# Kernel optimization log

Hardware: AMD Instinct MI355X
Metric: run time of the kernel (lower is better)

Reference implementation:

```python
import jax, jax.numpy as jnp
import numpy as np

N_NODES = 100000


def setup_inputs() -> dict:
    key = jax.random.key(0)
    k1, k2, k3, k4, k5 = jax.random.split(key, 5)
    n_feat, n_class = 128, 64
    E = 3200000
    x = jax.random.normal(k1, (N_NODES, n_feat), dtype=jnp.float32)
    edge_index = jax.random.randint(k2, (2, E), 0, N_NODES, dtype=jnp.int64)
    edge_weight = jax.random.uniform(k3, (E,), dtype=jnp.float32)
    # GCNConv params: glorot weight [in, out], zero-init bias (use small random for a non-trivial check)
    limit = float(np.sqrt(6.0 / (n_feat + n_class)))
    W = jax.random.uniform(k4, (n_feat, n_class), dtype=jnp.float32, minval=-limit, maxval=limit)
    b = jax.random.normal(k5, (n_class,), dtype=jnp.float32) * 0.01
    return {"x": x, "edge_index": edge_index, "edge_weight": edge_weight, "W": W, "b": b}


def _gcn_norm(edge_index, edge_weight, n):
    # add self-loops with weight 1 (PyG default fill_value=1.0)
    loop = jnp.arange(n, dtype=edge_index.dtype)
    row = jnp.concatenate([edge_index[0], loop])
    col = jnp.concatenate([edge_index[1], loop])
    w = jnp.concatenate([edge_weight, jnp.ones((n,), dtype=edge_weight.dtype)])
    deg = jax.ops.segment_sum(w, col, num_segments=n)  # in-degree by weight
    dis = jnp.where(deg > 0, jax.lax.rsqrt(jnp.where(deg > 0, deg, 1.0)), 0.0)
    norm = dis[row] * w * dis[col]
    return row, col, norm


def reference(x, edge_index, edge_weight, W, b):
    n = x.shape[0]
    row, col, norm = _gcn_norm(edge_index, edge_weight, n)
    h = x @ W  # linear transform before propagation, as in PyG GCNConv
    # gather source messages, scale by norm, scatter-add into targets
    msgs = h[row] * norm[:, None]          # [E+N, n_class]
    out = jax.ops.segment_sum(msgs, col, num_segments=n)
    return jax.nn.sigmoid(out + b)
```

## Files before the change

kernel.cpp:

```cpp
#include <hip/hip_runtime.h>
#include <hip/hip_bf16.h>
#include <math.h>


#define BLK 256
#define BBLK 1024
#define ABLK 1024
#define NBINBLK 512
#define NGRP 8
#define NB  512
#define CAPG 1024
#define CPB_MAX 200
#define PAD 76

typedef unsigned long long u64;
typedef unsigned int u32;
typedef unsigned short u16;
typedef unsigned char u8;
typedef _Float16 half8 __attribute__((ext_vector_type(8)));
typedef float f32x4 __attribute__((ext_vector_type(4)));

__global__ __launch_bounds__(BLK) void k_prep(const float* __restrict__ W,
                                              u16* __restrict__ WT,
                                              u32* __restrict__ cursor) {
    int gid = blockIdx.x * BLK + threadIdx.x;
    int gsz = gridDim.x * BLK;
    for (int i = gid; i < NB * NGRP; i += gsz) cursor[i] = 0u;
    for (int i = gid; i < 64 * 128; i += gsz) {
        int nn = i >> 7, k = i & 127;
        _Float16 h = (_Float16)W[k * 64 + nn];
        WT[nn * 128 + k] = *(u16*)&h;
    }
}

__global__ __launch_bounds__(BBLK) void k_bin(const int* __restrict__ row,
                                              const int* __restrict__ col,
                                              const float* __restrict__ w,
                                              u32* cursor,
                                              u64* __restrict__ staged,
                                              int E, int cpb, int nbins, int bpb) {
    __shared__ u32 hist[NB];
    __shared__ u32 sbase[NB];
    int t = threadIdx.x;
    int grp = blockIdx.x & (NGRP - 1);
    for (int j = t; j < NB; j += BBLK) hist[j] = 0;
    __syncthreads();
    int e0 = blockIdx.x * bpb;
    int e1 = min(e0 + bpb, E);
    int e = e0 + t;
    for (; e + 3 * BBLK < e1; e += 4 * BBLK) {
        int c0 = col[e];
        int c1 = col[e + BBLK];
        int c2 = col[e + 2 * BBLK];
        int c3 = col[e + 3 * BBLK];
        atomicAdd(&hist[(u32)c0 / (u32)cpb], 1u);
        atomicAdd(&hist[(u32)c1 / (u32)cpb], 1u);
        atomicAdd(&hist[(u32)c2 / (u32)cpb], 1u);
        atomicAdd(&hist[(u32)c3 / (u32)cpb], 1u);
    }
    for (; e < e1; e += BBLK)
        atomicAdd(&hist[(u32)col[e] / (u32)cpb], 1u);
    __syncthreads();
    for (int j = t; j < nbins; j += BBLK) {
        u32 h = hist[j];
        sbase[j] = h ? atomicAdd(&cursor[j * NGRP + grp], h) : 0u;
        hist[j] = 0u;
    }
    __syncthreads();
    e = e0 + t;
    for (; e + 3 * BBLK < e1; e += 4 * BBLK) {
#pragma unroll
        for (int j = 0; j < 4; j++) {
            int ee = e + j * BBLK;
            u32 c = (u32)col[ee];
            u32 bin = c / (u32)cpb;
            u32 colrel = c - bin * (u32)cpb;
            u32 wfix = (u32)(w[ee] * 65535.0f + 0.5f);
            u32 rel = sbase[bin] + atomicAdd(&hist[bin], 1u);
            if (rel < (u32)CAPG)
                staged[((size_t)bin * NGRP + grp) * CAPG + rel] =
                    (u64)((u32)row[ee] & 0xFFFFFu) | ((u64)colrel << 20)
                    | ((u64)wfix << 32);
        }
    }
    for (; e < e1; e += BBLK) {
        u32 c = (u32)col[e];
        u32 bin = c / (u32)cpb;
        u32 colrel = c - bin * (u32)cpb;
        u32 wfix = (u32)(w[e] * 65535.0f + 0.5f);
        u32 rel = sbase[bin] + atomicAdd(&hist[bin], 1u);
        if (rel < (u32)CAPG)
            staged[((size_t)bin * NGRP + grp) * CAPG + rel] =
                (u64)((u32)row[e] & 0xFFFFFu) | ((u64)colrel << 20)
                | ((u64)wfix << 32);
    }
}

__global__ __launch_bounds__(BLK) void k_deg(const u32* __restrict__ cursor,
                                             const u64* __restrict__ staged,
                                             float* __restrict__ dis,
                                             int N, int cpb) {
    __shared__ u32 deg[CPB_MAX];
    int bin = blockIdx.x, t = threadIdx.x;
    if (t < CPB_MAX) deg[t] = 0u;
    __syncthreads();
    for (int g = 0; g < NGRP; g++) {
        int ne = min((int)cursor[bin * NGRP + g], CAPG);
        size_t base = ((size_t)bin * NGRP + g) * CAPG;
        for (int i = t; i < ne; i += BLK) {
            u64 s = staged[base + i];
            atomicAdd(&deg[(u32)(s >> 20) & 0xFFFu], (u32)(s >> 32));
        }
    }
    __syncthreads();
    for (int j = t; j < cpb; j += BLK) {
        int c = bin * cpb + j;
        if (c < N)
            dis[c] = rsqrtf(1.0f + (float)deg[j] * (1.0f / 65535.0f));
    }
}

static __device__ __forceinline__ u16 f2bf(float f) {
    __hip_bfloat16 h = __float2bfloat16(f);
    return *(u16*)&h;
}

__global__ __launch_bounds__(BLK) void k_gemmM(const float* __restrict__ x,
                                               const u16* __restrict__ WT,
                                               const float* __restrict__ dis,
                                               u16* __restrict__ hs, int n) {
    __shared__ __attribute__((aligned(16))) _Float16 sx[64 * 136];
    __shared__ __attribute__((aligned(16))) _Float16 sw[64 * 136];
    __shared__ float sdis[64];
    int t = threadIdx.x;
    int m0 = blockIdx.x * 64;
    for (int i = t; i < 2048; i += BLK) {
        int r = i >> 5, q = i & 31;
        int gr = m0 + r;
        float4 v = make_float4(0.f, 0.f, 0.f, 0.f);
        if (gr < n) v = ((const float4*)x)[(size_t)gr * 32 + q];
        _Float16* dst = &sx[r * 136 + q * 4];
        dst[0] = (_Float16)v.x; dst[1] = (_Float16)v.y;
        dst[2] = (_Float16)v.z; dst[3] = (_Float16)v.w;
    }
    for (int i = t; i < 2048; i += BLK) {
        int nn = i >> 5, q = i & 31;
        ushort4 v = ((const ushort4*)WT)[nn * 32 + q];
        u16* dst = (u16*)&sw[nn * 136 + q * 4];
        dst[0] = v.x; dst[1] = v.y; dst[2] = v.z; dst[3] = v.w;
    }
    if (t < 64) sdis[t] = (m0 + t < n) ? dis[m0 + t] : 0.f;
    __syncthreads();
    int wv = t >> 6, lane = t & 63;
    int quad = lane >> 4, l16 = lane & 15;
    int mrow = wv * 16 + l16;
    half8 af[4];
#pragma unroll
    for (int kt = 0; kt < 4; kt++)
        af[kt] = *(const half8*)&sx[mrow * 136 + kt * 32 + quad * 8];
#pragma unroll
    for (int n0t = 0; n0t < 4; n0t++) {
        f32x4 acc = {0.f, 0.f, 0.f, 0.f};
#pragma unroll
        for (int kt = 0; kt < 4; kt++) {
            half8 bf_ = *(const half8*)&sw[(n0t * 16 + l16) * 136 + kt * 32 + quad * 8];
            acc = __builtin_amdgcn_mfma_f32_16x16x32_f16(af[kt], bf_, acc, 0, 0, 0);
        }
#pragma unroll
        for (int r = 0; r < 4; r++) {
            int mr = wv * 16 + quad * 4 + r;
            int gr = m0 + mr;
            if (gr < n)
                hs[(size_t)gr * 64 + n0t * 16 + l16] = f2bf(acc[r] * sdis[mr]);
        }
    }
}

__global__ __launch_bounds__(ABLK) void k_buildagg(const u32* __restrict__ cursor,
                                                   const u64* __restrict__ staged,
                                                   const uint2* __restrict__ hs64,
                                                   const float* __restrict__ dis,
                                                   const float* __restrict__ b,
                                                   float* __restrict__ out,
                                                   int N, int cpb) {
    __shared__ u32 cnt[CPB_MAX];
    __shared__ u32 lbkt[CPB_MAX * PAD];
    int bin = blockIdx.x, t = threadIdx.x;
    if (t < CPB_MAX) cnt[t] = 0u;
    __syncthreads();
    for (int g = 0; g < NGRP; g++) {
        int ne = min((int)cursor[bin * NGRP + g], CAPG);
        size_t base = ((size_t)bin * NGRP + g) * CAPG;
        for (int i = t; i < ne; i += ABLK) {
            u64 s = staged[base + i];
            u32 colrel = (u32)(s >> 20) & 0xFFFu;
            u32 wfix = (u32)(s >> 32);
            u32 rk = atomicAdd(&cnt[colrel], 1u);
            if (rk < (u32)PAD)
                lbkt[colrel * PAD + rk] = ((u32)s & 0xFFFFFu) | ((wfix >> 1) << 17);
        }
    }
    __syncthreads();
    int wv = t >> 6;
    int lane = t & 63;
    int q = lane >> 4, fp = lane & 15;
    const float WS = 1.0f / 32767.0f;
    for (int colrel = wv; colrel < cpb; colrel += (ABLK / 64)) {
        int node = bin * cpb + colrel;
        if (node >= N) break;
        int cc = (int)cnt[colrel];
        if (cc > PAD) cc = PAD;
        const u32* bkt = &lbkt[colrel * PAD];
        float a0, a1, a2, a3;
        if (q == 0) {
            uint2 s = hs64[((size_t)node << 4) + fp];
            a0 = __uint_as_float(s.x << 16);
            a1 = __uint_as_float(s.x & 0xFFFF0000u);
            a2 = __uint_as_float(s.y << 16);
            a3 = __uint_as_float(s.y & 0xFFFF0000u);
        } else {
            a0 = a1 = a2 = a3 = 0.f;
        }
        for (int e = 0; e < cc; e += 4) {
            int idx = e + q;
            u32 p = (idx < cc) ? bkt[idx] : 0u;
            float w = (float)(p >> 17) * WS;
            uint2 g = hs64[((size_t)(p & 0x1FFFFu) << 4) + fp];
            a0 = fmaf(__uint_as_float(g.x << 16), w, a0);
            a1 = fmaf(__uint_as_float(g.x & 0xFFFF0000u), w, a1);
            a2 = fmaf(__uint_as_float(g.y << 16), w, a2);
            a3 = fmaf(__uint_as_float(g.y & 0xFFFF0000u), w, a3);
        }
        a0 += __shfl_down(a0, 16); a1 += __shfl_down(a1, 16);
        a2 += __shfl_down(a2, 16); a3 += __shfl_down(a3, 16);
        a0 += __shfl_down(a0, 32); a1 += __shfl_down(a1, 32);
        a2 += __shfl_down(a2, 32); a3 += __shfl_down(a3, 32);
        if (q == 0) {
            float d = dis[node];
            float4 bv = ((const float4*)b)[fp];
            float4 o;
            o.x = 1.0f / (1.0f + __expf(-(d * a0 + bv.x)));
            o.y = 1.0f / (1.0f + __expf(-(d * a1 + bv.y)));
            o.z = 1.0f / (1.0f + __expf(-(d * a2 + bv.z)));
            o.w = 1.0f / (1.0f + __expf(-(d * a3 + bv.w)));
            ((float4*)out)[((size_t)node << 4) + fp] = o;
        }
    }
}

static inline size_t align_up(size_t v, size_t a) { return (v + a - 1) & ~(a - 1); }

extern "C" void kernel_launch(void* const* d_in, const int* in_sizes, int n_in,
                              void* d_out, int out_size, void* d_ws, size_t ws_size,
                              hipStream_t stream) {
    const float* x  = (const float*)d_in[0];
    const int*   ei = (const int*)d_in[1];
    const float* ew = (const float*)d_in[2];
    const float* W  = (const float*)d_in[3];
    const float* b  = (const float*)d_in[4];
    float* out = (float*)d_out;

    const int E = in_sizes[2];
    const int N = in_sizes[0] / 128;

    const int* row = ei;
    const int* col = ei + E;

    const int cpb   = (N + NB - 1) / NB;
    const int nbins = (N + cpb - 1) / cpb;
    const int bpb   = (E + NBINBLK - 1) / NBINBLK;

    char* p = (char*)d_ws;
    u32* cursor = (u32*)p; p += align_up((size_t)NB * NGRP * 4, 256);
    u64* staged = (u64*)p; p += align_up((size_t)NB * NGRP * CAPG * 8, 256);
    float* dis  = (float*)p; p += align_up((size_t)N * 4, 256);
    u16* hs     = (u16*)p; p += align_up((size_t)N * 64 * 2, 256);
    u16* WT     = (u16*)p; p += align_up((size_t)64 * 128 * 2, 256);
    (void)ws_size;

    k_prep<<<8, BLK, 0, stream>>>(W, WT, cursor);
    k_bin<<<NBINBLK, BBLK, 0, stream>>>(row, col, ew, cursor, staged,
                                        E, cpb, nbins, bpb);
    k_deg<<<nbins, BLK, 0, stream>>>(cursor, staged, dis, N, cpb);
    k_gemmM<<<(N + 63) / 64, BLK, 0, stream>>>(x, WT, dis, hs, N);
    k_buildagg<<<nbins, ABLK, 0, stream>>>(cursor, staged, (const uint2*)hs,
                                           dis, b, out, N, cpb);
}
```

Baseline: 268.2 us.

## Fold degree computation into binning and apply source normalization in aggregation

Removes the separate degree kernel: k_bin now accumulates per-node weighted degree with global atomics, and the GEMM no longer scales rows by the source normalization. The aggregation kernel computes rsqrt of the source degree per staged edge when building its local buckets, folds it into the quantized edge weight, and applies the destination normalization itself. A memset replaces the cursor-zeroing loop, and launch_bounds adds an occupancy hint to the aggregation kernel. This trades one kernel launch and one pass over staged edges for millions of global atomics and random degree reads in aggregation, and quantizing the combined weight can change precision.

```diff
diff --git a/kernel.cpp b/kernel.cpp
--- a/kernel.cpp
+++ b/kernel.cpp
@@ -16,20 +16,72 @@
 typedef unsigned long long u64;
 typedef unsigned int u32;
 typedef unsigned short u16;
-typedef unsigned char u8;
 typedef _Float16 half8 __attribute__((ext_vector_type(8)));
 typedef float f32x4 __attribute__((ext_vector_type(4)));
 
+static __device__ __forceinline__ u16 f2bf(float f) {
+    __hip_bfloat16 h = __float2bfloat16(f);
+    return *(u16*)&h;
+}
+static __device__ __forceinline__ float bfl(u32 v) { return __uint_as_float(v << 16); }
+static __device__ __forceinline__ float bfh(u32 v) { return __uint_as_float(v & 0xFFFF0000u); }
+
 __global__ __launch_bounds__(BLK) void k_prep(const float* __restrict__ W,
-                                              u16* __restrict__ WT,
-                                              u32* __restrict__ cursor) {
+                                              u16* __restrict__ WT) {
     int gid = blockIdx.x * BLK + threadIdx.x;
     int gsz = gridDim.x * BLK;
-    for (int i = gid; i < NB * NGRP; i += gsz) cursor[i] = 0u;
     for (int i = gid; i < 64 * 128; i += gsz) {
         int nn = i >> 7, k = i & 127;
         _Float16 h = (_Float16)W[k * 64 + nn];
         WT[nn * 128 + k] = *(u16*)&h;
+    }
+}
+
+__global__ __launch_bounds__(BLK) void k_gemmU(const float* __restrict__ x,
+                                               const u16* __restrict__ WT,
+                                               u16* __restrict__ hs, int n) {
+    __shared__ __attribute__((aligned(16))) _Float16 sx[64 * 136];
+    __shared__ __attribute__((aligned(16))) _Float16 sw[64 * 136];
+    int t = threadIdx.x;
+    int m0 = blockIdx.x * 64;
+    for (int i = t; i < 2048; i += BLK) {
+        int r = i >> 5, q = i & 31;
+        int gr = m0 + r;
+        float4 v = make_float4(0.f, 0.f, 0.f, 0.f);
+        if (gr < n) v = ((const float4*)x)[(size_t)gr * 32 + q];
+        _Float16* dst = &sx[r * 136 + q * 4];
+        dst[0] = (_Float16)v.x; dst[1] = (_Float16)v.y;
+        dst[2] = (_Float16)v.z; dst[3] = (_Float16)v.w;
+    }
+    for (int i = t; i < 2048; i += BLK) {
+        int nn = i >> 5, q = i & 31;
+        ushort4 v = ((const ushort4*)WT)[nn * 32 + q];
+        u16* dst = (u16*)&sw[nn * 136 + q * 4];
+        dst[0] = v.x; dst[1] = v.y; dst[2] = v.z; dst[3] = v.w;
+    }
+    __syncthreads();
+    int wv = t >> 6, lane = t & 63;
+    int quad = lane >> 4, l16 = lane & 15;
+    int mrow = wv * 16 + l16;
+    half8 af[4];
+#pragma unroll
+    for (int kt = 0; kt < 4; kt++)
+        af[kt] = *(const half8*)&sx[mrow * 136 + kt * 32 + quad * 8];
+#pragma unroll
+    for (int n0t = 0; n0t < 4; n0t++) {
+        f32x4 acc = {0.f, 0.f, 0.f, 0.f};
+#pragma unroll
+        for (int kt = 0; kt < 4; kt++) {
+            half8 bf_ = *(const half8*)&sw[(n0t * 16 + l16) * 136 + kt * 32 + quad * 8];
+            acc = __builtin_amdgcn_mfma_f32_16x16x32_f16(af[kt], bf_, acc, 0, 0, 0);
+        }
+#pragma unroll
+        for (int r = 0; r < 4; r++) {
+            int mr = wv * 16 + quad * 4 + r;
+            int gr = m0 + mr;
+            if (gr < n)
+                hs[(size_t)gr * 64 + n0t * 16 + l16] = f2bf(acc[r]);
+        }
     }
 }
 
@@ -38,6 +90,7 @@
                                               const float* __restrict__ w,
                                               u32* cursor,
                                               u64* __restrict__ staged,
+                                              u32* __restrict__ deg,
                                               int E, int cpb, int nbins, int bpb) {
     __shared__ u32 hist[NB];
     __shared__ u32 sbase[NB];
@@ -76,6 +129,7 @@
             u32 bin = c / (u32)cpb;
             u32 colrel = c - bin * (u32)cpb;
             u32 wfix = (u32)(w[ee] * 65535.0f + 0.5f);
+            atomicAdd(&deg[c], wfix);
             u32 rel = sbase[bin] + atomicAdd(&hist[bin], 1u);
             if (rel < (u32)CAPG)
                 staged[((size_t)bin * NGRP + grp) * CAPG + rel] =
@@ -88,6 +142,7 @@
         u32 bin = c / (u32)cpb;
         u32 colrel = c - bin * (u32)cpb;
         u32 wfix = (u32)(w[e] * 65535.0f + 0.5f);
+        atomicAdd(&deg[c], wfix);
         u32 rel = sbase[bin] + atomicAdd(&hist[bin], 1u);
         if (rel < (u32)CAPG)
             staged[((size_t)bin * NGRP + grp) * CAPG + rel] =
@@ -96,95 +151,16 @@
     }
 }
 
-__global__ __launch_bounds__(BLK) void k_deg(const u32* __restrict__ cursor,
-                                             const u64* __restrict__ staged,
-                                             float* __restrict__ dis,
-                                             int N, int cpb) {
-    __shared__ u32 deg[CPB_MAX];
-    int bin = blockIdx.x, t = threadIdx.x;
-    if (t < CPB_MAX) deg[t] = 0u;
-    __syncthreads();
-    for (int g = 0; g < NGRP; g++) {
-        int ne = min((int)cursor[bin * NGRP + g], CAPG);
-        size_t base = ((size_t)bin * NGRP + g) * CAPG;
-        for (int i = t; i < ne; i += BLK) {
-            u64 s = staged[base + i];
-            atomicAdd(&deg[(u32)(s >> 20) & 0xFFFu], (u32)(s >> 32));
-        }
-    }
-    __syncthreads();
-    for (int j = t; j < cpb; j += BLK) {
-        int c = bin * cpb + j;
-        if (c < N)
-            dis[c] = rsqrtf(1.0f + (float)deg[j] * (1.0f / 65535.0f));
-    }
-}
-
-static __device__ __forceinline__ u16 f2bf(float f) {
-    __hip_bfloat16 h = __float2bfloat16(f);
-    return *(u16*)&h;
-}
-
-__global__ __launch_bounds__(BLK) void k_gemmM(const float* __restrict__ x,
-                                               const u16* __restrict__ WT,
-                                               const float* __restrict__ dis,
-                                               u16* __restrict__ hs, int n) {
-    __shared__ __attribute__((aligned(16))) _Float16 sx[64 * 136];
-    __shared__ __attribute__((aligned(16))) _Float16 sw[64 * 136];
-    __shared__ float sdis[64];
-    int t = threadIdx.x;
-    int m0 = blockIdx.x * 64;
-    for (int i = t; i < 2048; i += BLK) {
-        int r = i >> 5, q = i & 31;
-        int gr = m0 + r;
-        float4 v = make_float4(0.f, 0.f, 0.f, 0.f);
-        if (gr < n) v = ((const float4*)x)[(size_t)gr * 32 + q];
-        _Float16* dst = &sx[r * 136 + q * 4];
-        dst[0] = (_Float16)v.x; dst[1] = (_Float16)v.y;
-        dst[2] = (_Float16)v.z; dst[3] = (_Float16)v.w;
-    }
-    for (int i = t; i < 2048; i += BLK) {
-        int nn = i >> 5, q = i & 31;
-        ushort4 v = ((const ushort4*)WT)[nn * 32 + q];
-        u16* dst = (u16*)&sw[nn * 136 + q * 4];
-        dst[0] = v.x; dst[1] = v.y; dst[2] = v.z; dst[3] = v.w;
-    }
-    if (t < 64) sdis[t] = (m0 + t < n) ? dis[m0 + t] : 0.f;
-    __syncthreads();
-    int wv = t >> 6, lane = t & 63;
-    int quad = lane >> 4, l16 = lane & 15;
-    int mrow = wv * 16 + l16;
-    half8 af[4];
-#pragma unroll
-    for (int kt = 0; kt < 4; kt++)
-        af[kt] = *(const half8*)&sx[mrow * 136 + kt * 32 + quad * 8];
-#pragma unroll
-    for (int n0t = 0; n0t < 4; n0t++) {
-        f32x4 acc = {0.f, 0.f, 0.f, 0.f};
-#pragma unroll
-        for (int kt = 0; kt < 4; kt++) {
-            half8 bf_ = *(const half8*)&sw[(n0t * 16 + l16) * 136 + kt * 32 + quad * 8];
-            acc = __builtin_amdgcn_mfma_f32_16x16x32_f16(af[kt], bf_, acc, 0, 0, 0);
-        }
-#pragma unroll
-        for (int r = 0; r < 4; r++) {
-            int mr = wv * 16 + quad * 4 + r;
-            int gr = m0 + mr;
-            if (gr < n)
-                hs[(size_t)gr * 64 + n0t * 16 + l16] = f2bf(acc[r] * sdis[mr]);
-        }
-    }
-}
-
-__global__ __launch_bounds__(ABLK) void k_buildagg(const u32* __restrict__ cursor,
-                                                   const u64* __restrict__ staged,
-                                                   const uint2* __restrict__ hs64,
-                                                   const float* __restrict__ dis,
-                                                   const float* __restrict__ b,
-                                                   float* __restrict__ out,
-                                                   int N, int cpb) {
+__global__ __launch_bounds__(ABLK, 8) void k_agg(const u32* __restrict__ cursor,
+                                                 const u64* __restrict__ staged,
+                                                 const uint2* __restrict__ hs64,
+                                                 const u32* __restrict__ deg,
+                                                 const float* __restrict__ b,
+                                                 float* __restrict__ out,
+                                                 int N, int cpb) {
     __shared__ u32 cnt[CPB_MAX];
     __shared__ u32 lbkt[CPB_MAX * PAD];
+    const float DS = 1.0f / 65535.0f;
     int bin = blockIdx.x, t = threadIdx.x;
     if (t < CPB_MAX) cnt[t] = 0u;
     __syncthreads();
@@ -194,10 +170,13 @@
         for (int i = t; i < ne; i += ABLK) {
             u64 s = staged[base + i];
             u32 colrel = (u32)(s >> 20) & 0xFFFu;
-            u32 wfix = (u32)(s >> 32);
+            u32 rowid = (u32)s & 0xFFFFFu;
+            float dr = rsqrtf(1.0f + (float)deg[rowid] * DS);
+            float wp = (float)(u32)(s >> 32) * DS * dr;
+            u32 q15 = (u32)(wp * 32767.0f + 0.5f);
             u32 rk = atomicAdd(&cnt[colrel], 1u);
             if (rk < (u32)PAD)
-                lbkt[colrel * PAD + rk] = ((u32)s & 0xFFFFFu) | ((wfix >> 1) << 17);
+                lbkt[colrel * PAD + rk] = rowid | (q15 << 17);
         }
     }
     __syncthreads();
@@ -211,13 +190,14 @@
         int cc = (int)cnt[colrel];
         if (cc > PAD) cc = PAD;
         const u32* bkt = &lbkt[colrel * PAD];
+        float dnode = rsqrtf(1.0f + (float)deg[node] * DS);
         float a0, a1, a2, a3;
         if (q == 0) {
             uint2 s = hs64[((size_t)node << 4) + fp];
-            a0 = __uint_as_float(s.x << 16);
-            a1 = __uint_as_float(s.x & 0xFFFF0000u);
-            a2 = __uint_as_float(s.y << 16);
-            a3 = __uint_as_float(s.y & 0xFFFF0000u);
+            a0 = bfl(s.x) * dnode;
+            a1 = bfh(s.x) * dnode;
+            a2 = bfl(s.y) * dnode;
+            a3 = bfh(s.y) * dnode;
         } else {
             a0 = a1 = a2 = a3 = 0.f;
         }
@@ -226,23 +206,22 @@
             u32 p = (idx < cc) ? bkt[idx] : 0u;
             float w = (float)(p >> 17) * WS;
             uint2 g = hs64[((size_t)(p & 0x1FFFFu) << 4) + fp];
-            a0 = fmaf(__uint_as_float(g.x << 16), w, a0);
-            a1 = fmaf(__uint_as_float(g.x & 0xFFFF0000u), w, a1);
-            a2 = fmaf(__uint_as_float(g.y << 16), w, a2);
-            a3 = fmaf(__uint_as_float(g.y & 0xFFFF0000u), w, a3);
+            a0 = fmaf(bfl(g.x), w, a0);
+            a1 = fmaf(bfh(g.x), w, a1);
+            a2 = fmaf(bfl(g.y), w, a2);
+            a3 = fmaf(bfh(g.y), w, a3);
         }
         a0 += __shfl_down(a0, 16); a1 += __shfl_down(a1, 16);
         a2 += __shfl_down(a2, 16); a3 += __shfl_down(a3, 16);
         a0 += __shfl_down(a0, 32); a1 += __shfl_down(a1, 32);
         a2 += __shfl_down(a2, 32); a3 += __shfl_down(a3, 32);
         if (q == 0) {
-            float d = dis[node];
             float4 bv = ((const float4*)b)[fp];
             float4 o;
-            o.x = 1.0f / (1.0f + __expf(-(d * a0 + bv.x)));
-            o.y = 1.0f / (1.0f + __expf(-(d * a1 + bv.y)));
-            o.z = 1.0f / (1.0f + __expf(-(d * a2 + bv.z)));
-            o.w = 1.0f / (1.0f + __expf(-(d * a3 + bv.w)));
+            o.x = 1.0f / (1.0f + __expf(-(dnode * a0 + bv.x)));
+            o.y = 1.0f / (1.0f + __expf(-(dnode * a1 + bv.y)));
+            o.z = 1.0f / (1.0f + __expf(-(dnode * a2 + bv.z)));
+            o.w = 1.0f / (1.0f + __expf(-(dnode * a3 + bv.w)));
             ((float4*)out)[((size_t)node << 4) + fp] = o;
         }
     }
@@ -269,20 +248,22 @@
     const int cpb   = (N + NB - 1) / NB;
     const int nbins = (N + cpb - 1) / cpb;
     const int bpb   = (E + NBINBLK - 1) / NBINBLK;
+    const int ntiles = (N + 63) / 64;
 
     char* p = (char*)d_ws;
     u32* cursor = (u32*)p; p += align_up((size_t)NB * NGRP * 4, 256);
+    u32* deg    = (u32*)p; p += align_up((size_t)N * 4, 256);
     u64* staged = (u64*)p; p += align_up((size_t)NB * NGRP * CAPG * 8, 256);
-    float* dis  = (float*)p; p += align_up((size_t)N * 4, 256);
     u16* hs     = (u16*)p; p += align_up((size_t)N * 64 * 2, 256);
     u16* WT     = (u16*)p; p += align_up((size_t)64 * 128 * 2, 256);
     (void)ws_size;
 
-    k_prep<<<8, BLK, 0, stream>>>(W, WT, cursor);
-    k_bin<<<NBINBLK, BBLK, 0, stream>>>(row, col, ew, cursor, staged,
+    hipMemsetAsync(cursor, 0,
+                   align_up((size_t)NB * NGRP * 4, 256) + (size_t)N * 4, stream);
+    k_prep<<<8, BLK, 0, stream>>>(W, WT);
+    k_gemmU<<<ntiles, BLK, 0, stream>>>(x, WT, hs, N);
+    k_bin<<<NBINBLK, BBLK, 0, stream>>>(row, col, ew, cursor, staged, deg,
                                         E, cpb, nbins, bpb);
-    k_deg<<<nbins, BLK, 0, stream>>>(cursor, staged, dis, N, cpb);
-    k_gemmM<<<(N + 63) / 64, BLK, 0, stream>>>(x, WT, dis, hs, N);
-    k_buildagg<<<nbins, ABLK, 0, stream>>>(cursor, staged, (const uint2*)hs,
-                                           dis, b, out, N, cpb);
-}
+    k_agg<<<nbins, ABLK, 0, stream>>>(cursor, staged, (const uint2*)hs,
+                                      deg, b, out, N, cpb);
+}
```

Result: slower. 357.6 us (+33.3%).
